# Optimization experiments

Hardware: AMD Instinct MI355X
Metric: run time of the kernel (lower is better)

The kernel has to match this reference:

```python
import jax, jax.numpy as jnp
import numpy as np

N_NODES = 50000
N_EDGES = 1250000
D_FEAT = 64
HIDDEN = 64


def setup_inputs() -> dict:
    key = jax.random.key(0)
    ks = jax.random.split(key, 6)
    state = jax.random.normal(ks[0], (N_NODES, D_FEAT), dtype=jnp.float32)
    ind = jax.random.randint(ks[1], (N_EDGES, 2), 0, N_NODES, dtype=jnp.int64)
    # scalar -> scalar interaction MLP (N_weights hidden units)
    w1 = jax.random.normal(ks[2], (HIDDEN,), dtype=jnp.float32)
    b1 = jax.random.normal(ks[3], (HIDDEN,), dtype=jnp.float32)
    w2 = jax.random.normal(ks[4], (HIDDEN,), dtype=jnp.float32) / np.sqrt(HIDDEN)
    b2 = jnp.zeros((1,), dtype=jnp.float32)
    return {"state": state, "ind": ind, "w1": w1, "b1": b1, "w2": w2, "b2": b2}


def _interaction(s, w1, b1, w2, b2):
    # s: [E] edge dot-products -> dE/ds: [E]
    h = jax.nn.gelu(s[:, None] * w1[None, :] + b1)  # [E, H]
    return h @ w2 + b2[0]  # [E]


def reference(state, ind, w1, b1, w2, b2):
    # normalize node states onto the unit sphere
    state = state / jnp.linalg.norm(state, axis=1, keepdims=True)  # [N, d]
    src = state[ind[:, 0]]  # [E, d] gather
    dst = state[ind[:, 1]]  # [E, d] gather
    s = jnp.sum(src * dst, axis=1)  # [E] edge dot product
    dE_ds = _interaction(s, w1, b1, w2, b2)[:, None]  # [E, 1]
    state_ = jnp.zeros_like(state)
    state_ = state_.at[ind[:, 0]].add(dE_ds * dst)  # scatter-add messages
    state_ = state_.at[ind[:, 1]].add(dE_ds * src)
    # project gradient flow onto tangent space of the sphere (negated)
    state_ = -state_ + state * jnp.sum(state * state_, axis=1, keepdims=True)
    return state_
```

## Files before the change

kernel.cpp:

```cpp
#include <hip/hip_runtime.h>


#define D 64
#define CAP 96
#define NSLICE 8
#define TAB 512
#define NPBIN 256
#define MAXBIN 256
#define SEGCAP 48
#define SCAP 14336
#define BINB 1024
#define TNODES 64

typedef _Float16 h8 __attribute__((ext_vector_type(8)));
typedef _Float16 h2 __attribute__((ext_vector_type(2)));
typedef float    f8 __attribute__((ext_vector_type(8)));
typedef int      i4 __attribute__((ext_vector_type(4)));
typedef unsigned int u4 __attribute__((ext_vector_type(4)));

#if __has_builtin(__builtin_amdgcn_fdot2)
#define FDOT2(a, b, c) __builtin_amdgcn_fdot2((a), (b), (c), false)
#else
#define FDOT2(a, b, c) fmaf((float)(a)[0], (float)(b)[0], \
                       fmaf((float)(a)[1], (float)(b)[1], (c)))
#endif


__device__ __forceinline__ float grpReduce8(float v) {
    v += __shfl_xor(v, 1, 64);
    v += __shfl_xor(v, 2, 64);
    v += __shfl_xor(v, 4, 64);
    return v;
}

__device__ __forceinline__ float grpReduce16(float v) {
    v += __shfl_xor(v, 1, 64);
    v += __shfl_xor(v, 2, 64);
    v += __shfl_xor(v, 4, 64);
    v += __shfl_xor(v, 8, 64);
    return v;
}

__device__ __forceinline__ float waveReduceSum64(float v) {
    v += __shfl_xor(v, 32, 64);
    v += __shfl_xor(v, 16, 64);
    v += __shfl_xor(v, 8, 64);
    v += __shfl_xor(v, 4, 64);
    v += __shfl_xor(v, 2, 64);
    v += __shfl_xor(v, 1, 64);
    return v;
}

__device__ __forceinline__ float dot4(float4 a, float4 b) {
    return fmaf(a.x, b.x, fmaf(a.y, b.y, fmaf(a.z, b.z, a.w * b.w)));
}

__device__ __forceinline__ float gelu_tanh(float x) {
    float u = -1.5957691216057308f * fmaf(0.044715f * x, x * x, x);
    float e = __expf(u);
    return x * __builtin_amdgcn_rcpf(1.0f + e);
}


__global__ void __launch_bounds__(256) prep_kernel(
        const float4* __restrict__ state4,
        h8* __restrict__ nh,
        int* __restrict__ gtail,
        unsigned int* __restrict__ streams,
        const long long* __restrict__ ind_ll,
        const float* __restrict__ w1,
        const float* __restrict__ b1,
        const float* __restrict__ w2,
        const float* __restrict__ b2,
        float2* __restrict__ table2,
        int n_nodes, int n_edges, int norm_blocks, int nbin) {
    __shared__ int scnt[MAXBIN];
    __shared__ int sbase[MAXBIN];
    __shared__ unsigned int seg[MAXBIN * SEGCAP];

    int bid = blockIdx.x;
    int tid = threadIdx.x;

    if (bid < norm_blocks) {
        int row = bid * 32 + (tid >> 3);
        int gl  = tid & 7;
        if (row < n_nodes) {
            float4 va = state4[(size_t)row * 16 + 2 * gl];
            float4 vb = state4[(size_t)row * 16 + 2 * gl + 1];
            float ss = grpReduce8(dot4(va, va) + dot4(vb, vb));
            float inv = 1.0f / sqrtf(ss);
            h8 hv;
            hv[0] = (_Float16)(va.x * inv); hv[1] = (_Float16)(va.y * inv);
            hv[2] = (_Float16)(va.z * inv); hv[3] = (_Float16)(va.w * inv);
            hv[4] = (_Float16)(vb.x * inv); hv[5] = (_Float16)(vb.y * inv);
            hv[6] = (_Float16)(vb.z * inv); hv[7] = (_Float16)(vb.w * inv);
            nh[(size_t)row * 8 + gl] = hv;
        }
        return;
    }

    if (bid < norm_blocks + 2) {
        int i = (bid - norm_blocks) * 256 + tid;
        if (i < TAB) {
            const float step = 2.0f / (float)(TAB - 1);
            float s0 = fmaf((float)i, step, -1.0f);
            float s1 = s0 + step;
            float f0 = b2[0], f1 = f0;
            for (int d = 0; d < D; ++d) {
                float w1d = w1[d], b1d = b1[d], w2d = w2[d];
                f0 += gelu_tanh(fmaf(s0, w1d, b1d)) * w2d;
                f1 += gelu_tanh(fmaf(s1, w1d, b1d)) * w2d;
            }
            table2[i] = make_float2(f0, f1 - f0);
        }
        return;
    }

    int b = bid - norm_blocks - 2;
    for (int i = tid; i < nbin; i += 256) scnt[i] = 0;
    __syncthreads();

    auto put = [&](int a, int c) {
        int bin = (unsigned)a >> 8;
        unsigned int rec = ((unsigned)(a & 255) << 16) | (unsigned)c;
        int q = atomicAdd(&scnt[bin], 1);
        if (q < SEGCAP) {
            seg[bin * SEGCAP + q] = rec;
        } else {
            int g = atomicAdd(&gtail[bin * 16], 1);
            if (g < SCAP) streams[(size_t)bin * SCAP + g] = rec;
        }
    };

    int P  = n_edges >> 1;
    int p0 = (int)((long long)P * b / BINB);
    int p1 = (int)((long long)P * (b + 1) / BINB);
    const i4* ind4 = (const i4*)ind_ll;

    for (int i = p0 + tid; i < p1; i += 256) {
        i4 e2 = __builtin_nontemporal_load(ind4 + i);
        put(e2.x, e2.y);
        put(e2.y, e2.x);
        put(e2.z, e2.w);
        put(e2.w, e2.z);
    }
    if (b == 0 && tid == 0 && (n_edges & 1)) {
        long long p = ind_ll[n_edges - 1];
        int a = (int)p, c = (int)(p >> 32);
        put(a, c);
        put(c, a);
    }
    __syncthreads();

    for (int s = tid; s < nbin; s += 256) {
        int cc = min(scnt[s], SEGCAP);
        sbase[s] = atomicAdd(&gtail[s * 16], cc);
    }
    __syncthreads();

    int wid = tid >> 6, lane = tid & 63;
    for (int s = wid; s < nbin; s += 4) {
        int cc = min(scnt[s], SEGCAP);
        int base = sbase[s];
        for (int i = lane; i < cc; i += 64) {
            int g = base + i;
            if (g < SCAP) streams[(size_t)s * SCAP + g] = seg[s * SEGCAP + i];
        }
    }
}


__global__ void __launch_bounds__(256) scatter_lds_kernel(
        const unsigned int* __restrict__ streams,
        const int* __restrict__ gtail,
        int* __restrict__ deg,
        unsigned int* __restrict__ entries_u32,
        int n_nodes, int nbin) {
    __shared__ int cur[TNODES];
    __shared__ unsigned short ent[TNODES * CAP];

    int blk = blockIdx.x;
    int bin = blk >> 2;
    int q   = blk & 3;
    int tid = threadIdx.x;
    int base_node = bin * NPBIN + q * TNODES;

    for (int i = tid; i < TNODES; i += 256) cur[i] = 0;
    __syncthreads();

    int cnt = min(gtail[bin * 16], SCAP);
    const unsigned int* sb = streams + (size_t)bin * SCAP;

    auto handle = [&](unsigned int rec) {
        int local = (int)(rec >> 16);
        if ((local >> 6) == q) {
            int r = local & 63;
            int slot = atomicAdd(&cur[r], 1);
            if (slot < CAP) ent[r * CAP + slot] = (unsigned short)(rec & 0xffffu);
        }
    };

    int cnt4 = cnt >> 2;
    const u4* sb4 = (const u4*)sb;
    for (int i = tid; i < cnt4; i += 256) {
        u4 r4 = sb4[i];
        handle(r4.x); handle(r4.y); handle(r4.z); handle(r4.w);
    }
    for (int i = (cnt4 << 2) + tid; i < cnt; i += 256) handle(sb[i]);
    __syncthreads();

    const unsigned int* ent32 = (const unsigned int*)ent;
    unsigned int* gdst = entries_u32 + (size_t)base_node * (CAP / 2);
    const int total32 = TNODES * CAP / 2;
    const int per_row32 = CAP / 2;
    for (int i = tid; i < total32; i += 256) {
        int row = i / per_row32;
        if (base_node + row < n_nodes) gdst[i] = ent32[i];
    }
    if (tid < TNODES) {
        int node = base_node + tid;
        if (node < n_nodes) deg[node] = min(cur[tid], CAP);
    }
}


__global__ void __launch_bounds__(256, 4) accum_kernel(
        const h8* __restrict__ nh,
        const int* __restrict__ deg,
        const unsigned short* __restrict__ entries,
        const float2* __restrict__ table2,
        float4* __restrict__ out4, int n_nodes, int slice_n) {
    int bid = blockIdx.x;
    int wid = threadIdx.x >> 6;
    int slice = bid & (NSLICE - 1);
    int local = (bid >> 3) * 4 + wid;
    if (local >= slice_n) return;
    int node = slice * slice_n + local;
    if (node >= n_nodes) return;

    int lane = threadIdx.x & 63;
    int grp  = lane >> 2;
    int gl   = lane & 3;

    h8 my0 = nh[(size_t)node * 8 + 2 * gl];
    h8 my1 = nh[(size_t)node * 8 + 2 * gl + 1];
    const h2* ma0 = (const h2*)&my0;
    const h2* ma1 = (const h2*)&my1;

    int dg = min(deg[node], CAP);
    const unsigned short* ebase = entries + (size_t)node * CAP;

    int ea = (int)ebase[lane];
    int eb = (int)ebase[64 + (lane & 31)];

    const float TS = 0.5f * (float)(TAB - 1);
    const float TMAX = (float)(TAB - 1) - 0.001f;

    f8 acc0 = {0.f, 0.f, 0.f, 0.f, 0.f, 0.f, 0.f, 0.f};
    f8 acc1 = {0.f, 0.f, 0.f, 0.f, 0.f, 0.f, 0.f, 0.f};

    int iters = (dg + 15) >> 4;

    int src0 = grp;
    int e0 = (src0 < 64) ? __shfl(ea, src0, 64) : __shfl(eb, src0 - 64, 64);
    int nbr0 = (src0 < dg) ? e0 : node;
    h8 cx0 = nh[(size_t)nbr0 * 8 + 2 * gl];
    h8 cx1 = nh[(size_t)nbr0 * 8 + 2 * gl + 1];
    bool cvalid = src0 < dg;

    for (int it = 0; it < iters; ++it) {
        h8 xh0 = cx0;
        h8 xh1 = cx1;
        bool valid = cvalid;

        int nsrc = (it + 1) * 16 + grp;
        if (it + 1 < iters) {
            int ne = (nsrc < 64) ? __shfl(ea, nsrc, 64) : __shfl(eb, nsrc - 64, 64);
            int nn = (nsrc < dg) ? ne : node;
            cx0 = nh[(size_t)nn * 8 + 2 * gl];
            cx1 = nh[(size_t)nn * 8 + 2 * gl + 1];
            cvalid = nsrc < dg;
        }

        const h2* xa0 = (const h2*)&xh0;
        const h2* xa1 = (const h2*)&xh1;

        float p = 0.f;
        #pragma unroll
        for (int j = 0; j < 4; ++j) {
            p = FDOT2(ma0[j], xa0[j], p);
            p = FDOT2(ma1[j], xa1[j], p);
        }
        p += __shfl_xor(p, 1, 64);
        p += __shfl_xor(p, 2, 64);

        float u = fmaf(p, TS, TS);
        u = fminf(fmaxf(u, 0.0f), TMAX);
        int i0 = (int)u;
        float fr = u - (float)i0;
        float2 t = table2[i0];
        float dE = fmaf(fr, t.y, t.x);
        if (!valid) dE = 0.0f;

        #pragma unroll
        for (int q = 0; q < 8; ++q) {
            acc0[q] = fmaf(dE, (float)xh0[q], acc0[q]);
            acc1[q] = fmaf(dE, (float)xh1[q], acc1[q]);
        }
    }

    #pragma unroll
    for (int q = 0; q < 8; ++q) {
        float t0 = acc0[q];
        t0 += __shfl_xor(t0, 4, 64);  t0 += __shfl_xor(t0, 8, 64);
        t0 += __shfl_xor(t0, 16, 64); t0 += __shfl_xor(t0, 32, 64);
        acc0[q] = t0;
        float t1 = acc1[q];
        t1 += __shfl_xor(t1, 4, 64);  t1 += __shfl_xor(t1, 8, 64);
        t1 += __shfl_xor(t1, 16, 64); t1 += __shfl_xor(t1, 32, 64);
        acc1[q] = t1;
    }

    float p2 = 0.f;
    #pragma unroll
    for (int q = 0; q < 8; ++q) {
        p2 = fmaf((float)my0[q], acc0[q], p2);
        p2 = fmaf((float)my1[q], acc1[q], p2);
    }
    p2 += __shfl_xor(p2, 1, 64);
    p2 += __shfl_xor(p2, 2, 64);
    float d2 = p2;

    if (grp == 0) {
        float4 r0, r1, r2, r3;
        r0.x = fmaf((float)my0[0], d2, -acc0[0]); r0.y = fmaf((float)my0[1], d2, -acc0[1]);
        r0.z = fmaf((float)my0[2], d2, -acc0[2]); r0.w = fmaf((float)my0[3], d2, -acc0[3]);
        r1.x = fmaf((float)my0[4], d2, -acc0[4]); r1.y = fmaf((float)my0[5], d2, -acc0[5]);
        r1.z = fmaf((float)my0[6], d2, -acc0[6]); r1.w = fmaf((float)my0[7], d2, -acc0[7]);
        r2.x = fmaf((float)my1[0], d2, -acc1[0]); r2.y = fmaf((float)my1[1], d2, -acc1[1]);
        r2.z = fmaf((float)my1[2], d2, -acc1[2]); r2.w = fmaf((float)my1[3], d2, -acc1[3]);
        r3.x = fmaf((float)my1[4], d2, -acc1[4]); r3.y = fmaf((float)my1[5], d2, -acc1[5]);
        r3.z = fmaf((float)my1[6], d2, -acc1[6]); r3.w = fmaf((float)my1[7], d2, -acc1[7]);
        size_t base = (size_t)node * 16 + 4 * gl;
        out4[base + 0] = r0;
        out4[base + 1] = r1;
        out4[base + 2] = r2;
        out4[base + 3] = r3;
    }
}


__global__ void norm_f32_kernel(const float4* __restrict__ state4,
                                float4* __restrict__ nstate4, int n_nodes) {
    int gid = blockIdx.x * blockDim.x + threadIdx.x;
    int row = gid >> 4;
    int gl  = threadIdx.x & 15;
    if (row >= n_nodes) return;
    float4 v = state4[row * 16 + gl];
    float ss = grpReduce16(dot4(v, v));
    float inv = 1.0f / sqrtf(ss);
    float4 r = {v.x * inv, v.y * inv, v.z * inv, v.w * inv};
    nstate4[row * 16 + gl] = r;
}

__global__ void edge_kernel(const float* __restrict__ nstate,
                            const int* __restrict__ ind,
                            const float* __restrict__ w1,
                            const float* __restrict__ b1,
                            const float* __restrict__ w2,
                            const float* __restrict__ b2,
                            float* __restrict__ acc, int n_edges) {
    int gid = blockIdx.x * blockDim.x + threadIdx.x;
    int edge = gid >> 6;
    int lane = threadIdx.x & 63;
    if (edge >= n_edges) return;
    const int2 e = ((const int2*)ind)[edge];
    float sv = nstate[e.x * D + lane];
    float dv = nstate[e.y * D + lane];
    float s = waveReduceSum64(sv * dv);
    float x = fmaf(s, w1[lane], b1[lane]);
    float h = gelu_tanh(x) * w2[lane];
    float dE = waveReduceSum64(h) + b2[0];
    atomicAdd(&acc[e.x * D + lane], dE * dv);
    atomicAdd(&acc[e.y * D + lane], dE * sv);
}

__global__ void final_kernel(const float* __restrict__ nstate,
                             float* __restrict__ out, int n_nodes) {
    int gid = blockIdx.x * blockDim.x + threadIdx.x;
    int row = gid >> 6;
    int lane = threadIdx.x & 63;
    if (row >= n_nodes) return;
    float a = out[row * D + lane];
    float n = nstate[row * D + lane];
    float dot = waveReduceSum64(n * a);
    out[row * D + lane] = fmaf(n, dot, -a);
}


extern "C" void kernel_launch(void* const* d_in, const int* in_sizes, int n_in,
                              void* d_out, int out_size, void* d_ws, size_t ws_size,
                              hipStream_t stream) {
    const float* state = (const float*)d_in[0];
    const int*   ind   = (const int*)d_in[1];
    const float* w1    = (const float*)d_in[2];
    const float* b1    = (const float*)d_in[3];
    const float* w2    = (const float*)d_in[4];
    const float* b2    = (const float*)d_in[5];

    int n_nodes = in_sizes[0] / D;
    int n_edges = in_sizes[1] / 2;
    int slice_n = (n_nodes + NSLICE - 1) / NSLICE;
    int nbin    = (n_nodes + NPBIN - 1) / NPBIN;

    size_t nh_bytes      = (size_t)n_nodes * D * 2;
    size_t gtail_off     = (nh_bytes + 255) & ~(size_t)255;
    size_t gtail_bytes   = ((size_t)nbin * 64 + 255) & ~(size_t)255;
    size_t deg_off       = gtail_off + gtail_bytes;
    size_t deg_bytes     = ((size_t)n_nodes * 4 + 255) & ~(size_t)255;
    size_t entries_off   = deg_off + deg_bytes;
    size_t entries_bytes = (size_t)n_nodes * CAP * 2;
    size_t table_off     = (entries_off + entries_bytes + 255) & ~(size_t)255;
    size_t table_bytes   = (size_t)TAB * sizeof(float2);
    size_t stream_off    = (table_off + table_bytes + 255) & ~(size_t)255;
    size_t stream_bytes  = (size_t)nbin * SCAP * 4;
    size_t needed        = stream_off + stream_bytes;

    const int threads = 256;

    if (ws_size >= needed && n_nodes <= 65535) {
        h8*             nh      = (h8*)d_ws;
        int*            gtail   = (int*)((char*)d_ws + gtail_off);
        int*            deg     = (int*)((char*)d_ws + deg_off);
        unsigned short* entries = (unsigned short*)((char*)d_ws + entries_off);
        float2*         table2  = (float2*)((char*)d_ws + table_off);
        unsigned int*   streams = (unsigned int*)((char*)d_ws + stream_off);

        hipMemsetAsync(gtail, 0, (size_t)nbin * 64, stream);

        int norm_blocks = (n_nodes + 31) / 32;
        int grid = norm_blocks + 2 + BINB;
        prep_kernel<<<grid, threads, 0, stream>>>(
            (const float4*)state, nh, gtail, streams,
            (const long long*)ind, w1, b1, w2, b2, table2,
            n_nodes, n_edges, norm_blocks, nbin);

        scatter_lds_kernel<<<nbin * 4, threads, 0, stream>>>(
            streams, gtail, deg, (unsigned int*)entries, n_nodes, nbin);

        int acc_blocks = NSLICE * ((slice_n + 3) / 4);
        accum_kernel<<<acc_blocks, threads, 0, stream>>>(
            nh, deg, entries, table2, (float4*)d_out, n_nodes, slice_n);
    } else {
        float* nstate = (float*)d_ws;
        hipMemsetAsync(d_out, 0, (size_t)out_size * sizeof(float), stream);
        int norm_blocks = (n_nodes * 16 + threads - 1) / threads;
        norm_f32_kernel<<<norm_blocks, threads, 0, stream>>>(
            (const float4*)state, (float4*)nstate, n_nodes);
        long long total = (long long)n_edges * D;
        int edge_blocks = (int)((total + threads - 1) / threads);
        edge_kernel<<<edge_blocks, threads, 0, stream>>>(
            nstate, ind, w1, b1, w2, b2, (float*)d_out, n_edges);
        int node_blocks = (n_nodes * D + threads - 1) / threads;
        final_kernel<<<node_blocks, threads, 0, stream>>>(nstate, (float*)d_out, n_nodes);
    }
}
```

Before: 109.1 us.

## Partition neighbor lists by index half to improve gather locality

The scatter kernel now splits each node's neighbor list into two segments, low-index neighbors filled from the front and high-index neighbors from the back, and packs both counts into deg. The accumulate kernel walks the two segments in turn, so gathers within each phase touch a narrower half of the node feature array, with the aim of better cache hit rates. The cost is an extra LDS counter, a second loop prologue with possibly wasted partial 16-wide iterations per segment, and more control flow.

```diff
diff --git a/kernel.cpp b/kernel.cpp
--- a/kernel.cpp
+++ b/kernel.cpp
@@ -175,8 +175,9 @@
         const int* __restrict__ gtail,
         int* __restrict__ deg,
         unsigned int* __restrict__ entries_u32,
-        int n_nodes, int nbin) {
-    __shared__ int cur[TNODES];
+        int n_nodes, int nbin, int half) {
+    __shared__ int cur_lo[TNODES];
+    __shared__ int cur_hi[TNODES];
     __shared__ unsigned short ent[TNODES * CAP];
 
     int blk = blockIdx.x;
@@ -185,7 +186,7 @@
     int tid = threadIdx.x;
     int base_node = bin * NPBIN + q * TNODES;
 
-    for (int i = tid; i < TNODES; i += 256) cur[i] = 0;
+    for (int i = tid; i < TNODES; i += 256) { cur_lo[i] = 0; cur_hi[i] = 0; }
     __syncthreads();
 
     int cnt = min(gtail[bin * 16], SCAP);
@@ -195,8 +196,15 @@
         int local = (int)(rec >> 16);
         if ((local >> 6) == q) {
             int r = local & 63;
-            int slot = atomicAdd(&cur[r], 1);
-            if (slot < CAP) ent[r * CAP + slot] = (unsigned short)(rec & 0xffffu);
+            int nbr = (int)(rec & 0xffffu);
+            if (nbr < half) {
+                int slot = atomicAdd(&cur_lo[r], 1);
+                if (slot < CAP) ent[r * CAP + slot] = (unsigned short)nbr;
+            } else {
+                int s = atomicAdd(&cur_hi[r], 1);
+                int slot = CAP - 1 - s;
+                if (slot >= 0) ent[r * CAP + slot] = (unsigned short)nbr;
+            }
         }
     };
 
@@ -219,7 +227,11 @@
     }
     if (tid < TNODES) {
         int node = base_node + tid;
-        if (node < n_nodes) deg[node] = min(cur[tid], CAP);
+        if (node < n_nodes) {
+            int lo = min(cur_lo[tid], CAP);
+            int hi = min(cur_hi[tid], CAP - lo);
+            deg[node] = lo | (hi << 16);
+        }
     }
 }
 
@@ -247,7 +259,12 @@
     const h2* ma0 = (const h2*)&my0;
     const h2* ma1 = (const h2*)&my1;
 
-    int dg = min(deg[node], CAP);
+    int dp  = deg[node];
+    int dlo = dp & 0xffff;
+    int dhi = (dp >> 16) & 0xffff;
+    dlo = min(dlo, CAP);
+    dhi = min(dhi, CAP - dlo);
+
     const unsigned short* ebase = entries + (size_t)node * CAP;
 
     int ea = (int)ebase[lane];
@@ -259,55 +276,64 @@
     f8 acc0 = {0.f, 0.f, 0.f, 0.f, 0.f, 0.f, 0.f, 0.f};
     f8 acc1 = {0.f, 0.f, 0.f, 0.f, 0.f, 0.f, 0.f, 0.f};
 
-    int iters = (dg + 15) >> 4;
-
-    int src0 = grp;
-    int e0 = (src0 < 64) ? __shfl(ea, src0, 64) : __shfl(eb, src0 - 64, 64);
-    int nbr0 = (src0 < dg) ? e0 : node;
-    h8 cx0 = nh[(size_t)nbr0 * 8 + 2 * gl];
-    h8 cx1 = nh[(size_t)nbr0 * 8 + 2 * gl + 1];
-    bool cvalid = src0 < dg;
-
-    for (int it = 0; it < iters; ++it) {
-        h8 xh0 = cx0;
-        h8 xh1 = cx1;
-        bool valid = cvalid;
-
-        int nsrc = (it + 1) * 16 + grp;
-        if (it + 1 < iters) {
-            int ne = (nsrc < 64) ? __shfl(ea, nsrc, 64) : __shfl(eb, nsrc - 64, 64);
-            int nn = (nsrc < dg) ? ne : node;
-            cx0 = nh[(size_t)nn * 8 + 2 * gl];
-            cx1 = nh[(size_t)nn * 8 + 2 * gl + 1];
-            cvalid = nsrc < dg;
-        }
-
-        const h2* xa0 = (const h2*)&xh0;
-        const h2* xa1 = (const h2*)&xh1;
-
-        float p = 0.f;
-        #pragma unroll
-        for (int j = 0; j < 4; ++j) {
-            p = FDOT2(ma0[j], xa0[j], p);
-            p = FDOT2(ma1[j], xa1[j], p);
-        }
-        p += __shfl_xor(p, 1, 64);
-        p += __shfl_xor(p, 2, 64);
-
-        float u = fmaf(p, TS, TS);
-        u = fminf(fmaxf(u, 0.0f), TMAX);
-        int i0 = (int)u;
-        float fr = u - (float)i0;
-        float2 t = table2[i0];
-        float dE = fmaf(fr, t.y, t.x);
-        if (!valid) dE = 0.0f;
-
-        #pragma unroll
-        for (int q = 0; q < 8; ++q) {
-            acc0[q] = fmaf(dE, (float)xh0[q], acc0[q]);
-            acc1[q] = fmaf(dE, (float)xh1[q], acc1[q]);
-        }
-    }
+    auto run_seg = [&](int b, int e) {
+        if (e <= b) return;
+        int b16 = b & ~15;
+        int iters = (e - b16 + 15) >> 4;
+
+        int src0 = b16 + grp;
+        int e0 = (src0 < 64) ? __shfl(ea, src0, 64) : __shfl(eb, src0 - 64, 64);
+        bool cvalid = (src0 >= b) && (src0 < e);
+        int nbr0 = cvalid ? e0 : node;
+        h8 cx0 = nh[(size_t)nbr0 * 8 + 2 * gl];
+        h8 cx1 = nh[(size_t)nbr0 * 8 + 2 * gl + 1];
+
+        for (int it = 0; it < iters; ++it) {
+            h8 xh0 = cx0;
+            h8 xh1 = cx1;
+            bool valid = cvalid;
+
+            int nsrc = b16 + (it + 1) * 16 + grp;
+            if (it + 1 < iters) {
+                int ne = (nsrc < 64) ? __shfl(ea, nsrc, 64)
+                                     : __shfl(eb, nsrc - 64, 64);
+                bool nv = (nsrc >= b) && (nsrc < e);
+                int nn = nv ? ne : node;
+                cx0 = nh[(size_t)nn * 8 + 2 * gl];
+                cx1 = nh[(size_t)nn * 8 + 2 * gl + 1];
+                cvalid = nv;
+            }
+
+            const h2* xa0 = (const h2*)&xh0;
+            const h2* xa1 = (const h2*)&xh1;
+
+            float p = 0.f;
+            #pragma unroll
+            for (int j = 0; j < 4; ++j) {
+                p = FDOT2(ma0[j], xa0[j], p);
+                p = FDOT2(ma1[j], xa1[j], p);
+            }
+            p += __shfl_xor(p, 1, 64);
+            p += __shfl_xor(p, 2, 64);
+
+            float u = fmaf(p, TS, TS);
+            u = fminf(fmaxf(u, 0.0f), TMAX);
+            int i0 = (int)u;
+            float fr = u - (float)i0;
+            float2 t = table2[i0];
+            float dE = fmaf(fr, t.y, t.x);
+            if (!valid) dE = 0.0f;
+
+            #pragma unroll
+            for (int q = 0; q < 8; ++q) {
+                acc0[q] = fmaf(dE, (float)xh0[q], acc0[q]);
+                acc1[q] = fmaf(dE, (float)xh1[q], acc1[q]);
+            }
+        }
+    };
+
+    run_seg(0, dlo);
+    run_seg(CAP - dhi, CAP);
 
     #pragma unroll
     for (int q = 0; q < 8; ++q) {
@@ -412,6 +438,7 @@
     int n_edges = in_sizes[1] / 2;
     int slice_n = (n_nodes + NSLICE - 1) / NSLICE;
     int nbin    = (n_nodes + NPBIN - 1) / NPBIN;
+    int half    = (n_nodes + 1) >> 1;
 
     size_t nh_bytes      = (size_t)n_nodes * D * 2;
     size_t gtail_off     = (nh_bytes + 255) & ~(size_t)255;
@@ -446,7 +473,7 @@
             n_nodes, n_edges, norm_blocks, nbin);
 
         scatter_lds_kernel<<<nbin * 4, threads, 0, stream>>>(
-            streams, gtail, deg, (unsigned int*)entries, n_nodes, nbin);
+            streams, gtail, deg, (unsigned int*)entries, n_nodes, nbin, half);
 
         int acc_blocks = NSLICE * ((slice_n + 3) / 4);
         accum_kernel<<<acc_blocks, threads, 0, stream>>>(
```

New measurement: 115.3 us. 5.7% more time.
